# Kernel tuning notes

Hardware: AMD Instinct MI355X
Metric: run time of the kernel (lower is better)

Reference implementation:

```python
import jax, jax.numpy as jnp
import numpy as np

B, C, F, T = 4, 64, 64, 128
IC = 32  # inter_channels = C // 2
EPS = 1e-5  # BatchNorm eps


def _conv1x1(x, w, b=None):
    # x: (B, Cin, H, W), w: (Cout, Cin)
    y = jnp.einsum('bchw,oc->bohw', x, w)
    if b is not None:
        y = y + b[None, :, None, None]
    return y


def _maxpool2(x):
    b, c, h, w = x.shape
    return x.reshape(b, c, h // 2, 2, w // 2, 2).max(axis=(3, 5))


def _pos_score(fsz, tsz, h2_w):
    # positional encoding is (fpos, tpos) in [0,1]; the 2->1 conv head makes the
    # pos_delta contribution separable: score(n,m) = s(n) - s(m)
    fpos = jnp.linspace(0.0, 1.0, fsz)
    tpos = jnp.linspace(0.0, 1.0, tsz)
    return (h2_w[0] * fpos[:, None] + h2_w[1] * tpos[None, :]).reshape(-1)


def setup_inputs() -> dict:
    key = jax.random.key(0)
    ks = jax.random.split(key, 16)
    s = 0.05
    inp = {
        'x': jax.random.normal(ks[0], (B, C, F, T), dtype=jnp.float32),
        'psi_w': jax.random.normal(ks[1], (IC, C)) * s,
        'psi_b': jax.random.normal(ks[2], (IC,)) * s,
        'theta_w': jax.random.normal(ks[3], (IC, C)) * s,
        'theta_b': jax.random.normal(ks[4], (IC,)) * s,
        'phi_w': jax.random.normal(ks[5], (IC, C)) * s,
        'phi_b': jax.random.normal(ks[6], (IC,)) * s,
        'h0_w': jax.random.normal(ks[7], (IC,)) * s,
        'h1_w': jax.random.normal(ks[8], (IC,)) * s,
        'h2_w': jax.random.normal(ks[9], (2,)) * s,
        'W_w': jax.random.normal(ks[10], (C, IC + 1)) * s,
        'W_b': jax.random.normal(ks[11], (C,)) * s,
        'bn_gamma': jax.random.normal(ks[12], (C,)) * s + 1.0,
        'bn_beta': jax.random.normal(ks[13], (C,)) * s,
        'bn_mean': jax.random.normal(ks[14], (C,)) * s,
        'bn_var': jax.random.uniform(ks[15], (C,), minval=0.5, maxval=1.5),
    }
    return inp


def reference(x, psi_w, psi_b, theta_w, theta_b, phi_w, phi_b,
              h0_w, h1_w, h2_w, W_w, W_b, bn_gamma, bn_beta, bn_mean, bn_var):
    Bs, Cs, Fs, Ts = x.shape
    N = Fs * Ts
    M = (Fs // 2) * (Ts // 2)

    psi_x = _maxpool2(_conv1x1(x, psi_w, psi_b))      # (B, IC, F/2, T/2)
    theta_x = _conv1x1(x, theta_w, theta_b)           # (B, IC, F, T)
    phi_x = _maxpool2(_conv1x1(x, phi_w, phi_b))      # (B, IC, F/2, T/2)

    # additive attention scores: relu(head0(theta) + head1(phi) + head2(pos_delta))
    t_score = jnp.einsum('bcft,c->bft', theta_x, h0_w).reshape(Bs, N)   # (B, N)
    p_score = jnp.einsum('bcft,c->bft', phi_x, h1_w).reshape(Bs, M)     # (B, M)
    a = _pos_score(Fs, Ts, h2_w)             # (N,) query pos contribution
    bpos = _pos_score(Fs // 2, Ts // 2, h2_w)  # (M,) key pos contribution
    f = jax.nn.relu((t_score + a[None, :])[:, :, None]
                    + (p_score - bpos[None, :])[:, None, :])  # (B, N, M)

    f_div = f / jnp.asarray(M, f.dtype)
    psi_flat = psi_x.reshape(Bs, IC, M)
    y = jnp.einsum('bnm,bcm->bcn', f_div, psi_flat).reshape(Bs, IC, Fs, Ts)

    # r_structure_type='zero' -> structure feature is zeros (1 extra channel)
    structure = jnp.zeros((Bs, 1, Fs, Ts), dtype=y.dtype)
    y = jnp.concatenate([y, structure], axis=1)       # (B, IC+1, F, T)

    wy = _conv1x1(y, W_w, W_b)                        # (B, C, F, T)
    inv = bn_gamma / jnp.sqrt(bn_var + EPS)
    wy = wy * inv[None, :, None, None] + (bn_beta - bn_mean * inv)[None, :, None, None]
    return wy + x
```

## Files before the change

kernel.cpp:

```cpp
#include <hip/hip_runtime.h>

#define B_ 4
#define C_ 64
#define F_ 64
#define T_ 128
#define IC_ 32
#define N_ 8192
#define M_ 2048

#define OFF_U      0
#define OFF_Z      32768
#define OFF_V      557056
#define OFF_VS     565248
#define OFF_Q01    573440
#define WS_FLOATS  1622528

__device__ __align__(16) float g_ws[WS_FLOATS];
__device__ int g_perm[B_ * M_];

typedef __attribute__((ext_vector_type(8))) short short8_t;
typedef __attribute__((ext_vector_type(4))) float f32x4;

__device__ __forceinline__ unsigned short f2bf(float f) {
    unsigned b = __float_as_uint(f);
    b += 0x7fffu + ((b >> 16) & 1u);
    return (unsigned short)(b >> 16);
}
__device__ __forceinline__ float bf2f(unsigned short h) {
    return __uint_as_float(((unsigned)h) << 16);
}

#define XSIDX(p, c)  ((((p) * 64) + (c)) ^ (((p) & 7) << 3))
#define WAIDX(o, c)  ((((o) * 64) + (c)) ^ (((o) & 7) << 3))
#define WZIDX(o, c)  ((((o) * 32) + (c)) ^ (((o) & 3) << 3))
#define PSIDX(p, c)  ((((p) * 32) + (c)) ^ (((p) & 3) << 3))

__global__ __launch_bounds__(256) void k1(
    const float* __restrict__ x,
    const float* __restrict__ psi_w, const float* __restrict__ psi_b,
    const float* __restrict__ theta_w, const float* __restrict__ theta_b,
    const float* __restrict__ phi_w, const float* __restrict__ phi_b,
    const float* __restrict__ h0_w, const float* __restrict__ h1_w,
    const float* __restrict__ h2_w, const float* __restrict__ W_w)
{
    float* __restrict__ ws = g_ws;
    __shared__ __align__(16) unsigned short XS[128 * 64];
    __shared__ __align__(16) unsigned short WA[64 * 64];
    __shared__ __align__(16) unsigned short WZ[64 * 32];
    __shared__ __align__(16) unsigned short PS[32 * 32];
    __shared__ __align__(16) float pb[64];
    __shared__ __align__(16) float h1l[32];
    __shared__ __align__(16) float wtl[64];
    __shared__ float vtmp[2][32];

    const int tid = threadIdx.x;
    const int bid = blockIdx.x;
    const int b = bid >> 6;
    const int rem = bid & 63;
    const int fh = rem >> 1;
    const int hf = rem & 1;

    const float h20 = h2_w[0], h21 = h2_w[1];

    for (int it = 0; it < 2; ++it) {
        const int u = it * 256 + tid;
        const int colq = u & 15, r = (u >> 4) & 1, cq = u >> 5;
        float4 xv[4];
#pragma unroll
        for (int j = 0; j < 4; ++j)
            xv[j] = *(const float4*)&x[(((size_t)b * 64 + (4 * cq + j)) * 64 + (2 * fh + r)) * 128 + hf * 64 + 4 * colq];
        const float* xf0 = (const float*)&xv[0];
        const float* xf1 = (const float*)&xv[1];
        const float* xf2 = (const float*)&xv[2];
        const float* xf3 = (const float*)&xv[3];
#pragma unroll
        for (int i = 0; i < 4; ++i) {
            const int p = r * 64 + 4 * colq + i;
            short4 sv;
            sv.x = (short)f2bf(xf0[i]); sv.y = (short)f2bf(xf1[i]);
            sv.z = (short)f2bf(xf2[i]); sv.w = (short)f2bf(xf3[i]);
            *(short4*)&XS[XSIDX(p, 4 * cq)] = sv;
        }
    }
    for (int it = 0; it < 4; ++it) {
        const int f4 = it * 256 + tid;
        const int o2 = f4 >> 4;
        const int cq = f4 & 15;
        const float* src = (o2 < 32) ? &psi_w[o2 * 64 + 4 * cq]
                                     : &phi_w[(o2 - 32) * 64 + 4 * cq];
        const float4 wv = *(const float4*)src;
        short4 sv;
        sv.x = (short)f2bf(wv.x); sv.y = (short)f2bf(wv.y);
        sv.z = (short)f2bf(wv.z); sv.w = (short)f2bf(wv.w);
        *(short4*)&WA[WAIDX(o2, 4 * cq)] = sv;
    }
    for (int it = 0; it < 8; ++it) {
        const int e = it * 256 + tid;
        const int o64 = e >> 5, ic = e & 31;
        WZ[WZIDX(o64, ic)] = f2bf(W_w[o64 * 33 + ic]);
    }
    if (tid < 64) pb[tid] = (tid < 32) ? psi_b[tid] : phi_b[tid - 32];
    if (tid < 32) h1l[tid] = h1_w[tid];
    if (tid < 64) {
        float acc = 0.f;
        for (int o2 = 0; o2 < 32; ++o2)
            acc += h0_w[o2] * theta_w[o2 * 64 + tid];
        wtl[tid] = acc;
    }
    __syncthreads();

    const int w = tid >> 6, lane = tid & 63;
    const int lo = lane & 15, hi = lane >> 4;

    short8_t a0 = *(const short8_t*)&WA[WAIDX(16 * w + lo, hi * 8)];
    short8_t a1 = *(const short8_t*)&WA[WAIDX(16 * w + lo, 32 + hi * 8)];
    f32x4 acc[8];
#pragma unroll
    for (int t = 0; t < 8; ++t) { acc[t].x = 0.f; acc[t].y = 0.f; acc[t].z = 0.f; acc[t].w = 0.f; }
#pragma unroll
    for (int t = 0; t < 8; ++t) {
        const short8_t b0 = *(const short8_t*)&XS[XSIDX(16 * t + lo, hi * 8)];
        const short8_t b1 = *(const short8_t*)&XS[XSIDX(16 * t + lo, 32 + hi * 8)];
        acc[t] = __builtin_amdgcn_mfma_f32_16x16x32_bf16(a0, b0, acc[t], 0, 0, 0);
        acc[t] = __builtin_amdgcn_mfma_f32_16x16x32_bf16(a1, b1, acc[t], 0, 0, 0);
    }

    const int isPsi = (w < 2);
    const int obase = (w & 1) * 16 + hi * 4;
    const int pcj = lo >> 1;
#pragma unroll
    for (int t = 0; t < 4; ++t) {
        const int pc = 8 * t + pcj;
        float pv[4];
#pragma unroll
        for (int r = 0; r < 4; ++r) {
            const float mx = fmaxf(acc[t][r], acc[t + 4][r]);
            pv[r] = fmaxf(mx, __shfl_xor(mx, 1, 64)) + pb[(isPsi ? 0 : 32) + obase + r];
        }
        if (isPsi) {
            if ((lane & 1) == 0) {
                short4 sv;
                sv.x = (short)f2bf(pv[0]); sv.y = (short)f2bf(pv[1]);
                sv.z = (short)f2bf(pv[2]); sv.w = (short)f2bf(pv[3]);
                *(short4*)&PS[PSIDX(pc, obase)] = sv;
            }
        } else {
            float hp = h1l[obase] * pv[0] + h1l[obase + 1] * pv[1]
                     + h1l[obase + 2] * pv[2] + h1l[obase + 3] * pv[3];
            hp += __shfl_xor(hp, 16, 64);
            hp += __shfl_xor(hp, 32, 64);
            if (hi == 0 && (lane & 1) == 0)
                vtmp[w - 2][pc] = hp;
        }
    }
    __syncthreads();

    if (tid < 32) {
        const int pc = tid;
        const int m = fh * 64 + hf * 32 + pc;
        const float bpos = h20 * (fh * (1.0f / 31.0f))
                         + h21 * ((hf * 32 + pc) * (1.0f / 63.0f));
        ws[OFF_V + b * 2048 + m] = vtmp[0][pc] + vtmp[1][pc] - bpos;
    }

    {
        const short8_t az = *(const short8_t*)&WZ[WZIDX(16 * w + lo, hi * 8)];
#pragma unroll
        for (int pt = 0; pt < 2; ++pt) {
            const short8_t bz = *(const short8_t*)&PS[PSIDX(16 * pt + lo, hi * 8)];
            f32x4 zc; zc.x = 0.f; zc.y = 0.f; zc.z = 0.f; zc.w = 0.f;
            zc = __builtin_amdgcn_mfma_f32_16x16x32_bf16(az, bz, zc, 0, 0, 0);
            const int m = fh * 64 + hf * 32 + 16 * pt + lo;
#pragma unroll
            for (int r = 0; r < 4; ++r)
                ws[OFF_Z + ((size_t)b * 64 + 16 * w + hi * 4 + r) * 2048 + m] = zc[r];
        }
    }

    {
        const int ph = tid & 1, p = tid >> 1;
        float ua = 0.f;
#pragma unroll
        for (int c4 = 0; c4 < 8; ++c4) {
            const int c = ph * 32 + c4 * 4;
            const short4 xv = *(const short4*)&XS[XSIDX(p, c)];
            const float4 wv = *(const float4*)&wtl[c];
            ua += wv.x * bf2f((unsigned short)xv.x) + wv.y * bf2f((unsigned short)xv.y)
                + wv.z * bf2f((unsigned short)xv.z) + wv.w * bf2f((unsigned short)xv.w);
        }
        ua += __shfl_xor(ua, 1, 64);
        if (ph == 0) {
            float tb_ = 0.f;
            for (int o2 = 0; o2 < 32; ++o2)
                tb_ += h0_w[o2] * theta_b[o2];
            const int f = 2 * fh + (p >> 6), tt = hf * 64 + (p & 63);
            const int n = f * 128 + tt;
            const float a = h20 * (f * (1.0f / 63.0f)) + h21 * (tt * (1.0f / 127.0f));
            ws[OFF_U + b * 8192 + n] = ua + tb_ + a;
        }
    }
}

__global__ __launch_bounds__(256) void k2()
{
    float* __restrict__ ws = g_ws;
    __shared__ __align__(16) float vl[2048];
    __shared__ int part[256];
    const int tid = threadIdx.x;
    const int b = blockIdx.x >> 7, chunk = blockIdx.x & 127;
    const float* v = ws + OFF_V + b * 2048;
    for (int i = tid; i < 2048; i += 256) vl[i] = v[i];
    __syncthreads();

    const int ml = tid >> 4;
    const int jq = tid & 15;
    const int m = chunk * 16 + ml;
    const float vm = vl[m];
    int cnt = 0;
    const float4* v4 = (const float4*)vl;
#pragma unroll 4
    for (int i = 0; i < 32; ++i) {
        const int j4 = jq + 16 * i;
        const float4 vv = v4[j4];
        const int jb = j4 * 4;
        cnt += (vv.x > vm) || (vv.x == vm && (jb    ) < m);
        cnt += (vv.y > vm) || (vv.y == vm && (jb + 1) < m);
        cnt += (vv.z > vm) || (vv.z == vm && (jb + 2) < m);
        cnt += (vv.w > vm) || (vv.w == vm && (jb + 3) < m);
    }
    part[tid] = cnt;
    __syncthreads();
    if (tid < 16) {
        int r = 0;
#pragma unroll
        for (int j = 0; j < 16; ++j) r += part[tid * 16 + j];
        ws[OFF_VS + b * 2048 + r] = vl[chunk * 16 + tid];
        g_perm[b * 2048 + r] = chunk * 16 + tid;
    }
}

__global__ __launch_bounds__(512) void k3()
{
    float* __restrict__ ws = g_ws;
    __shared__ float wt0[8], wt1[8];
    const int tid = threadIdx.x;
    const int b = blockIdx.x >> 6, o = blockIdx.x & 63;

    const int* perm = g_perm + b * 2048;
    const float* vs = ws + OFF_VS + b * 2048;
    const float* zg = ws + OFF_Z + ((size_t)b * 64 + o) * 2048;

    float zl[4], vlv[4];
    float s0 = 0.f, s1 = 0.f;
    const int base = tid * 4;
#pragma unroll
    for (int qq = 0; qq < 4; ++qq) {
        const int i = base + qq;
        const int mp = perm[i];
        const float z = zg[mp];
        const float vv = vs[i];
        zl[qq] = z; vlv[qq] = vv;
        s0 += z; s1 += vv * z;
    }

    float w0 = s0, w1 = s1;
    const int lane = tid & 63, wv = tid >> 6;
#pragma unroll
    for (int off = 1; off < 64; off <<= 1) {
        const float t0_ = __shfl_up(w0, off, 64);
        const float t1_ = __shfl_up(w1, off, 64);
        if (lane >= off) { w0 += t0_; w1 += t1_; }
    }
    if (lane == 63) { wt0[wv] = w0; wt1[wv] = w1; }
    __syncthreads();
    float base0 = 0.f, base1 = 0.f;
    for (int w = 0; w < wv; ++w) { base0 += wt0[w]; base1 += wt1[w]; }
    float r0 = w0 + base0 - s0, r1 = w1 + base1 - s1;

    float2* Q01 = (float2*)(ws + OFF_Q01) + (size_t)b * 2049 * 64;
#pragma unroll
    for (int qq = 0; qq < 4; ++qq) {
        r0 += zl[qq]; r1 += vlv[qq] * zl[qq];
        float2 p; p.x = r0; p.y = r1;
        Q01[(size_t)(base + qq + 1) * 64 + o] = p;
    }
    if (tid == 0) { float2 z2; z2.x = 0.f; z2.y = 0.f; Q01[o] = z2; }
}

__global__ __launch_bounds__(512) void k4(
    const float* __restrict__ x,
    const float* __restrict__ W_b,
    const float* __restrict__ bn_g, const float* __restrict__ bn_b,
    const float* __restrict__ bn_m, const float* __restrict__ bn_v,
    float* __restrict__ out)
{
    const float* __restrict__ ws = g_ws;
    __shared__ __align__(16) float vsl[2048];
    __shared__ float tileb[64 * 65];
    __shared__ int karr[64];
    __shared__ float uarr[64];

    const int tid = threadIdx.x;
    const int b = blockIdx.x >> 7, tile = blockIdx.x & 127;
    const int n0 = tile * 64;

    const float* vs = ws + OFF_VS + b * 2048;
    *(float4*)&vsl[tid * 4] = *(const float4*)&vs[tid * 4];
    __syncthreads();

    if (tid < 64) {
        const float u = ws[OFF_U + b * 8192 + n0 + tid];
        const float thr = -u;
        int lo = 0, hi = 2048;
        while (lo < hi) {
            const int mid = (lo + hi) >> 1;
            if (vsl[mid] > thr) lo = mid + 1; else hi = mid;
        }
        karr[tid] = lo;
        uarr[tid] = u;
    }
    __syncthreads();

    const int lane = tid & 63, w = tid >> 6;
    const float inv = bn_g[lane] * __frsqrt_rn(bn_v[lane] + 1e-5f);
    const float sft = W_b[lane] * inv + bn_b[lane] - bn_m[lane] * inv;
    const float2* Q01 = (const float2*)(ws + OFF_Q01) + (size_t)b * 2049 * 64;

    for (int nl = w; nl < 64; nl += 8) {
        const int k = karr[nl];
        const float u = uarr[nl];
        const float2 qv = Q01[(size_t)k * 64 + lane];
        const float raw = (u * qv.x + qv.y) * (1.0f / 2048.0f);
        tileb[lane * 65 + nl] = raw * inv + sft;
    }
    __syncthreads();

    for (int idx = tid; idx < 2048; idx += 512) {
        const int o = idx >> 5, j2 = idx & 31;
        const size_t gi = ((size_t)b * 64 + o) * 8192 + n0 + 2 * j2;
        const float2 xv = *(const float2*)&x[gi];
        float2 r;
        r.x = tileb[o * 65 + 2 * j2] + xv.x;
        r.y = tileb[o * 65 + 2 * j2 + 1] + xv.y;
        *(float2*)&out[gi] = r;
    }
}

extern "C" void kernel_launch(void* const* d_in, const int* in_sizes, int n_in,
                              void* d_out, int out_size, void* d_ws, size_t ws_size,
                              hipStream_t stream)
{
    (void)in_sizes; (void)n_in; (void)out_size; (void)d_ws; (void)ws_size;
    const float* x       = (const float*)d_in[0];
    const float* psi_w   = (const float*)d_in[1];
    const float* psi_b   = (const float*)d_in[2];
    const float* theta_w = (const float*)d_in[3];
    const float* theta_b = (const float*)d_in[4];
    const float* phi_w   = (const float*)d_in[5];
    const float* phi_b   = (const float*)d_in[6];
    const float* h0_w    = (const float*)d_in[7];
    const float* h1_w    = (const float*)d_in[8];
    const float* h2_w    = (const float*)d_in[9];
    const float* W_w     = (const float*)d_in[10];
    const float* W_b     = (const float*)d_in[11];
    const float* bn_g    = (const float*)d_in[12];
    const float* bn_b    = (const float*)d_in[13];
    const float* bn_m    = (const float*)d_in[14];
    const float* bn_v    = (const float*)d_in[15];
    float* out = (float*)d_out;

    k1<<<dim3(256), dim3(256), 0, stream>>>(x, psi_w, psi_b, theta_w, theta_b,
                                            phi_w, phi_b, h0_w, h1_w, h2_w, W_w);
    k2<<<dim3(512), dim3(256), 0, stream>>>();
    k3<<<dim3(256), dim3(512), 0, stream>>>();
    k4<<<dim3(512), dim3(512), 0, stream>>>(x, W_b, bn_g, bn_b, bn_m, bn_v, out);
}
```

Baseline: 113.5 us.

## Merge prefix-scan and output kernels with per-batch atomic flag handoff

```diff
diff --git a/kernel.cpp b/kernel.cpp
--- a/kernel.cpp
+++ b/kernel.cpp
@@ -17,6 +17,9 @@
 
 __device__ __align__(16) float g_ws[WS_FLOATS];
 __device__ int g_perm[B_ * M_];
+
+__device__ unsigned g_done[B_ * 64];
+__device__ unsigned g_cons[B_ * 64];
 
 typedef __attribute__((ext_vector_type(8))) short short8_t;
 typedef __attribute__((ext_vector_type(4))) float f32x4;
@@ -239,110 +242,123 @@
     }
 }
 
-__global__ __launch_bounds__(512) void k3()
-{
-    float* __restrict__ ws = g_ws;
-    __shared__ float wt0[8], wt1[8];
-    const int tid = threadIdx.x;
-    const int b = blockIdx.x >> 6, o = blockIdx.x & 63;
-
-    const int* perm = g_perm + b * 2048;
-    const float* vs = ws + OFF_VS + b * 2048;
-    const float* zg = ws + OFF_Z + ((size_t)b * 64 + o) * 2048;
-
-    float zl[4], vlv[4];
-    float s0 = 0.f, s1 = 0.f;
-    const int base = tid * 4;
-#pragma unroll
-    for (int qq = 0; qq < 4; ++qq) {
-        const int i = base + qq;
-        const int mp = perm[i];
-        const float z = zg[mp];
-        const float vv = vs[i];
-        zl[qq] = z; vlv[qq] = vv;
-        s0 += z; s1 += vv * z;
-    }
-
-    float w0 = s0, w1 = s1;
-    const int lane = tid & 63, wv = tid >> 6;
-#pragma unroll
-    for (int off = 1; off < 64; off <<= 1) {
-        const float t0_ = __shfl_up(w0, off, 64);
-        const float t1_ = __shfl_up(w1, off, 64);
-        if (lane >= off) { w0 += t0_; w1 += t1_; }
-    }
-    if (lane == 63) { wt0[wv] = w0; wt1[wv] = w1; }
-    __syncthreads();
-    float base0 = 0.f, base1 = 0.f;
-    for (int w = 0; w < wv; ++w) { base0 += wt0[w]; base1 += wt1[w]; }
-    float r0 = w0 + base0 - s0, r1 = w1 + base1 - s1;
-
-    float2* Q01 = (float2*)(ws + OFF_Q01) + (size_t)b * 2049 * 64;
-#pragma unroll
-    for (int qq = 0; qq < 4; ++qq) {
-        r0 += zl[qq]; r1 += vlv[qq] * zl[qq];
-        float2 p; p.x = r0; p.y = r1;
-        Q01[(size_t)(base + qq + 1) * 64 + o] = p;
-    }
-    if (tid == 0) { float2 z2; z2.x = 0.f; z2.y = 0.f; Q01[o] = z2; }
-}
-
-__global__ __launch_bounds__(512) void k4(
+__global__ __launch_bounds__(512) void k34(
     const float* __restrict__ x,
     const float* __restrict__ W_b,
     const float* __restrict__ bn_g, const float* __restrict__ bn_b,
     const float* __restrict__ bn_m, const float* __restrict__ bn_v,
     float* __restrict__ out)
 {
-    const float* __restrict__ ws = g_ws;
+    float* __restrict__ ws = g_ws;
     __shared__ __align__(16) float vsl[2048];
     __shared__ float tileb[64 * 65];
     __shared__ int karr[64];
     __shared__ float uarr[64];
+    __shared__ float wt0[8], wt1[8];
 
     const int tid = threadIdx.x;
-    const int b = blockIdx.x >> 7, tile = blockIdx.x & 127;
-    const int n0 = tile * 64;
-
-    const float* vs = ws + OFF_VS + b * 2048;
-    *(float4*)&vsl[tid * 4] = *(const float4*)&vs[tid * 4];
-    __syncthreads();
-
-    if (tid < 64) {
-        const float u = ws[OFF_U + b * 8192 + n0 + tid];
-        const float thr = -u;
-        int lo = 0, hi = 2048;
-        while (lo < hi) {
-            const int mid = (lo + hi) >> 1;
-            if (vsl[mid] > thr) lo = mid + 1; else hi = mid;
-        }
-        karr[tid] = lo;
-        uarr[tid] = u;
-    }
-    __syncthreads();
-
-    const int lane = tid & 63, w = tid >> 6;
-    const float inv = bn_g[lane] * __frsqrt_rn(bn_v[lane] + 1e-5f);
-    const float sft = W_b[lane] * inv + bn_b[lane] - bn_m[lane] * inv;
-    const float2* Q01 = (const float2*)(ws + OFF_Q01) + (size_t)b * 2049 * 64;
-
-    for (int nl = w; nl < 64; nl += 8) {
-        const int k = karr[nl];
-        const float u = uarr[nl];
-        const float2 qv = Q01[(size_t)k * 64 + lane];
-        const float raw = (u * qv.x + qv.y) * (1.0f / 2048.0f);
-        tileb[lane * 65 + nl] = raw * inv + sft;
-    }
-    __syncthreads();
-
-    for (int idx = tid; idx < 2048; idx += 512) {
-        const int o = idx >> 5, j2 = idx & 31;
-        const size_t gi = ((size_t)b * 64 + o) * 8192 + n0 + 2 * j2;
-        const float2 xv = *(const float2*)&x[gi];
-        float2 r;
-        r.x = tileb[o * 65 + 2 * j2] + xv.x;
-        r.y = tileb[o * 65 + 2 * j2 + 1] + xv.y;
-        *(float2*)&out[gi] = r;
+
+    if (blockIdx.x < 256) {
+        const int b = blockIdx.x >> 6, o = blockIdx.x & 63;
+
+        const int* perm = g_perm + b * 2048;
+        const float* vs = ws + OFF_VS + b * 2048;
+        const float* zg = ws + OFF_Z + ((size_t)b * 64 + o) * 2048;
+
+        float zl[4], vlv[4];
+        float s0 = 0.f, s1 = 0.f;
+        const int base = tid * 4;
+#pragma unroll
+        for (int qq = 0; qq < 4; ++qq) {
+            const int i = base + qq;
+            const int mp = perm[i];
+            const float z = zg[mp];
+            const float vv = vs[i];
+            zl[qq] = z; vlv[qq] = vv;
+            s0 += z; s1 += vv * z;
+        }
+
+        float w0 = s0, w1 = s1;
+        const int lane = tid & 63, wv = tid >> 6;
+#pragma unroll
+        for (int off = 1; off < 64; off <<= 1) {
+            const float t0_ = __shfl_up(w0, off, 64);
+            const float t1_ = __shfl_up(w1, off, 64);
+            if (lane >= off) { w0 += t0_; w1 += t1_; }
+        }
+        if (lane == 63) { wt0[wv] = w0; wt1[wv] = w1; }
+        __syncthreads();
+        float base0 = 0.f, base1 = 0.f;
+        for (int w = 0; w < wv; ++w) { base0 += wt0[w]; base1 += wt1[w]; }
+        float r0 = w0 + base0 - s0, r1 = w1 + base1 - s1;
+
+        float2* Q01 = (float2*)(ws + OFF_Q01) + (size_t)b * 2049 * 64;
+#pragma unroll
+        for (int qq = 0; qq < 4; ++qq) {
+            r0 += zl[qq]; r1 += vlv[qq] * zl[qq];
+            float2 p; p.x = r0; p.y = r1;
+            Q01[(size_t)(base + qq + 1) * 64 + o] = p;
+        }
+        if (tid == 0) { float2 z2; z2.x = 0.f; z2.y = 0.f; Q01[o] = z2; }
+
+        __syncthreads();
+        if (tid == 0)
+            __hip_atomic_fetch_add(&g_done[b * 64], 1u, __ATOMIC_ACQ_REL,
+                                   __HIP_MEMORY_SCOPE_AGENT);
+    } else {
+        const int idx = (int)blockIdx.x - 256;
+        const int b = idx >> 7, tile = idx & 127;
+        const int n0 = tile * 64;
+
+        const float* vs = ws + OFF_VS + b * 2048;
+        *(float4*)&vsl[tid * 4] = *(const float4*)&vs[tid * 4];
+        __syncthreads();
+
+        if (tid < 64) {
+            const float u = ws[OFF_U + b * 8192 + n0 + tid];
+            const float thr = -u;
+            int lo = 0, hi = 2048;
+            while (lo < hi) {
+                const int mid = (lo + hi) >> 1;
+                if (vsl[mid] > thr) lo = mid + 1; else hi = mid;
+            }
+            karr[tid] = lo;
+            uarr[tid] = u;
+        } else if (tid == 256) {
+            const unsigned t = __hip_atomic_fetch_add(&g_cons[b * 64], 1u,
+                                                      __ATOMIC_RELAXED,
+                                                      __HIP_MEMORY_SCOPE_AGENT);
+            const unsigned goal = ((t >> 7) + 1u) * 64u;
+            while (__hip_atomic_load(&g_done[b * 64], __ATOMIC_RELAXED,
+                                     __HIP_MEMORY_SCOPE_AGENT) < goal)
+                __builtin_amdgcn_s_sleep(8);
+            __builtin_amdgcn_fence(__ATOMIC_ACQUIRE, "agent");
+        }
+        __syncthreads();
+
+        const int lane = tid & 63, w = tid >> 6;
+        const float inv = bn_g[lane] * __frsqrt_rn(bn_v[lane] + 1e-5f);
+        const float sft = W_b[lane] * inv + bn_b[lane] - bn_m[lane] * inv;
+        const float2* Q01 = (const float2*)(ws + OFF_Q01) + (size_t)b * 2049 * 64;
+
+        for (int nl = w; nl < 64; nl += 8) {
+            const int k = karr[nl];
+            const float u = uarr[nl];
+            const float2 qv = Q01[(size_t)k * 64 + lane];
+            const float raw = (u * qv.x + qv.y) * (1.0f / 2048.0f);
+            tileb[lane * 65 + nl] = raw * inv + sft;
+        }
+        __syncthreads();
+
+        for (int i2 = tid; i2 < 2048; i2 += 512) {
+            const int o = i2 >> 5, j2 = i2 & 31;
+            const size_t gi = ((size_t)b * 64 + o) * 8192 + n0 + 2 * j2;
+            const float2 xv = *(const float2*)&x[gi];
+            float2 r;
+            r.x = tileb[o * 65 + 2 * j2] + xv.x;
+            r.y = tileb[o * 65 + 2 * j2 + 1] + xv.y;
+            *(float2*)&out[gi] = r;
+        }
     }
 }
 
@@ -372,6 +388,5 @@
     k1<<<dim3(256), dim3(256), 0, stream>>>(x, psi_w, psi_b, theta_w, theta_b,
                                             phi_w, phi_b, h0_w, h1_w, h2_w, W_w);
     k2<<<dim3(512), dim3(256), 0, stream>>>();
-    k3<<<dim3(256), dim3(512), 0, stream>>>();
-    k4<<<dim3(512), dim3(512), 0, stream>>>(x, W_b, bn_g, bn_b, bn_m, bn_v, out);
-}
+    k34<<<dim3(768), dim3(512), 0, stream>>>(x, W_b, bn_g, bn_b, bn_m, bn_v, out);
+}
```

New measurement: 132.4 us. +16.6%, slower.
